# Kernel tuning notes

Hardware: AMD Instinct MI355X
Metric: run time of the kernel (lower is better)

The kernel has to match this reference:

```python
import jax, jax.numpy as jnp
import numpy as np

N_NODES = 50000
N_EDGES = 800000
IN_DIM = 256
OUT_DIM = 64
HEADS = 4
NEG_SLOPE = 0.2  # PyG GATConv default


def setup_inputs() -> dict:
    key = jax.random.key(0)
    k_x, k_e, k_w, k_as, k_ad = jax.random.split(key, 5)
    x = jax.random.normal(k_x, (N_NODES, IN_DIM), dtype=jnp.float32)
    edge_index = jax.random.randint(k_e, (2, N_EDGES), 0, N_NODES, dtype=jnp.int64)
    # Glorot-ish scaled params (as in PyG GATConv)
    W = jax.random.normal(k_w, (IN_DIM, HEADS * OUT_DIM), dtype=jnp.float32) / np.sqrt(IN_DIM)
    att_src = jax.random.normal(k_as, (HEADS, OUT_DIM), dtype=jnp.float32) / np.sqrt(OUT_DIM)
    att_dst = jax.random.normal(k_ad, (HEADS, OUT_DIM), dtype=jnp.float32) / np.sqrt(OUT_DIM)
    bias = jnp.zeros((HEADS * OUT_DIM,), dtype=jnp.float32)
    return {"x": x, "edge_index": edge_index, "W": W,
            "att_src": att_src, "att_dst": att_dst, "bias": bias}


def reference(x, edge_index, W, att_src, att_dst, bias):
    N = x.shape[0]
    H, C = att_src.shape
    # add self-loops (PyG GATConv default add_self_loops=True)
    loop = jnp.arange(N, dtype=edge_index.dtype)
    src = jnp.concatenate([edge_index[0], loop])  # [E+N] message sources j
    dst = jnp.concatenate([edge_index[1], loop])  # [E+N] message targets i

    xh = (x @ W).reshape(N, H, C)                 # [N, H, C]
    a_src = jnp.einsum('nhc,hc->nh', xh, att_src)  # [N, H]
    a_dst = jnp.einsum('nhc,hc->nh', xh, att_dst)  # [N, H]

    logits = jax.nn.leaky_relu(a_src[src] + a_dst[dst], NEG_SLOPE)  # [E+N, H]
    # segment softmax over incoming edges of each destination node
    seg_max = jax.ops.segment_max(logits, dst, num_segments=N)      # [N, H]
    e = jnp.exp(logits - seg_max[dst])
    seg_sum = jax.ops.segment_sum(e, dst, num_segments=N)           # [N, H]
    alpha = e / seg_sum[dst]                                        # [E+N, H]

    # weighted scatter-aggregate of source features
    msgs = alpha[:, :, None] * xh[src]                              # [E+N, H, C]
    out = jax.ops.segment_sum(msgs, dst, num_segments=N)            # [N, H, C]
    out = out.reshape(N, H * C) + bias                              # concat heads + bias
    # h.dim() == 2 here, so the original's mean(dim=1) branch is not taken
    return out
```

## Files before the change

kernel.cpp:

```cpp
#include <hip/hip_runtime.h>

#define NEG_SLOPE 0.2f
#define LRELU(x) ((x) > 0.0f ? (x) : NEG_SLOPE * (x))

typedef short short8 __attribute__((ext_vector_type(8)));
typedef unsigned short ushort8 __attribute__((ext_vector_type(8)));
typedef float f32x4v __attribute__((ext_vector_type(4)));

__device__ __forceinline__ unsigned short f2bf(float f) {
  unsigned int u = __float_as_uint(f);
  unsigned int r = (u + 0x7FFFu + ((u >> 16) & 1u)) >> 16;
  return (unsigned short)r;
}

__device__ __forceinline__ float bf2f(unsigned short u) {
  return __uint_as_float(((unsigned int)u) << 16);
}

__device__ __forceinline__ unsigned int cvt_pk_bf16(float lo, float hi) {
  unsigned int r;
  asm("v_cvt_pk_bf16_f32 %0, %1, %2" : "=v"(r) : "v"(lo), "v"(hi));
  return r;
}

__device__ __forceinline__ void gload_lds16(const void* g, void* l) {
  __builtin_amdgcn_global_load_lds(
      (const __attribute__((address_space(1))) unsigned int*)g,
      (__attribute__((address_space(3))) unsigned int*)l, 16, 0, 0);
}

#define CBC 448
#define CBW 64
#define CBF 1024

__global__ __launch_bounds__(256) void fused_pre(
    const float* __restrict__ W, unsigned short* __restrict__ Wtb,
    const int* __restrict__ ei, int* __restrict__ deg,
    int* __restrict__ rank, int E) {
  int b = blockIdx.x;
  int tid = threadIdx.x;
  if (b < CBC) {
    for (int e = b * 256 + tid; e < E; e += CBC * 256)
      rank[e] = atomicAdd(&deg[ei[E + e]], 1);
  } else {
    int bb = b - CBC;
    for (int idx = bb * 256 + tid; idx < 256 * 256; idx += CBW * 256) {
      int n = idx >> 8, k = idx & 255;
      Wtb[n * 256 + k] = f2bf(W[k * 256 + n]);
    }
  }
}

__global__ __launch_bounds__(1024) void scan1_kernel(const int* __restrict__ deg,
                                                     int* __restrict__ row_start,
                                                     int* __restrict__ bsum, int N) {
  __shared__ int buf[1024];
  int i = blockIdx.x * 1024 + (int)threadIdx.x;
  int v = (i < N) ? deg[i] : 0;
  buf[threadIdx.x] = v;
  __syncthreads();
  int run = v;
  for (int off = 1; off < 1024; off <<= 1) {
    int t = ((int)threadIdx.x >= off) ? buf[threadIdx.x - off] : 0;
    __syncthreads();
    run += t;
    buf[threadIdx.x] = run;
    __syncthreads();
  }
  if (i < N) row_start[i] = run - v;
  if (threadIdx.x == 1023) bsum[blockIdx.x] = run;
}

__global__ __launch_bounds__(1024) void scan_off(int* __restrict__ row_start,
                                                 const int* __restrict__ bsum,
                                                 int nb, int N) {
  __shared__ int s_off;
  int b = blockIdx.x;
  if (threadIdx.x < 64) {
    int acc = 0;
    for (int j = (int)threadIdx.x; j < b; j += 64) acc += bsum[j];
    for (int off = 32; off; off >>= 1) acc += __shfl_down(acc, off, 64);
    if (threadIdx.x == 0) s_off = acc;
  }
  __syncthreads();
  int off = s_off;
  int i = b * 1024 + (int)threadIdx.x;
  if (i < N) row_start[i] += off;
  if (b == nb - 1 && threadIdx.x == 0) row_start[N] = off + bsum[b];
}

__global__ __launch_bounds__(256) void fused_main(
    const float* __restrict__ Xf, const unsigned short* __restrict__ Wtb,
    const float* __restrict__ attS, const float* __restrict__ attD,
    unsigned short* __restrict__ XHb, float* __restrict__ a_src,
    float* __restrict__ a_dst,
    const int* __restrict__ ei, const int* __restrict__ row_start,
    const int* __restrict__ rank, int* __restrict__ csr_src,
    int nGemm, int E, int N) {
  __shared__ unsigned short lA[128 * 32];
  __shared__ unsigned short lB[128 * 32];
  const int bid = blockIdx.x;
  const int tid = threadIdx.x;

  if (bid >= nGemm) {
    int bb = bid - nGemm;
    for (int e = bb * 256 + tid; e < E; e += CBF * 256)
      csr_src[row_start[ei[E + e]] + rank[e]] = ei[e];
    return;
  }

  const int gb = bid;
  const int lane = tid & 63;
  const int wave = tid >> 6;
  const int m0 = ((gb >> 4) * 8 + (gb & 7)) * 128;
  const int n0 = ((gb >> 3) & 1) * 128;
  const int wr = (wave >> 1) * 64;
  const int wc = (wave & 1) * 64;

  f32x4v acc[4][4];
#pragma unroll
  for (int i = 0; i < 4; ++i)
#pragma unroll
    for (int j = 0; j < 4; ++j) acc[i][j] = (f32x4v)(0.0f);

  const int srow = tid >> 2;
  const int skb = (tid & 3) * 16;
  const float* ap0 = Xf + (size_t)min(m0 + (tid >> 2), N - 1) * 256 + (tid & 3) * 8;
  const float* ap1 = Xf + (size_t)min(m0 + 64 + (tid >> 2), N - 1) * 256 + (tid & 3) * 8;

  const char* WtC = (const char*)Wtb;
  char* lAc = (char*)&lA[0];
  char* lBc = (char*)&lB[0];
  const int ldsB0 = wave * 1024;
  const int lr = lane & 15;
  const int hq = lane >> 4;
  const int kq = hq * 16;

  float4 c0 = *reinterpret_cast<const float4*>(ap0);
  float4 c1 = *reinterpret_cast<const float4*>(ap0 + 4);
  float4 c2 = *reinterpret_cast<const float4*>(ap1);
  float4 c3 = *reinterpret_cast<const float4*>(ap1 + 4);

#pragma unroll
  for (int kk = 0; kk < 8; ++kk) {
    const int k0 = kk * 32;
    gload_lds16(WtC + (size_t)(n0 + srow) * 512 + (size_t)k0 * 2 + skb, lBc + ldsB0);
    gload_lds16(WtC + (size_t)(n0 + srow + 64) * 512 + (size_t)k0 * 2 + skb,
                lBc + ldsB0 + 4096);
    {
      uint4 w0, w1;
      w0.x = cvt_pk_bf16(c0.x, c0.y); w0.y = cvt_pk_bf16(c0.z, c0.w);
      w0.z = cvt_pk_bf16(c1.x, c1.y); w0.w = cvt_pk_bf16(c1.z, c1.w);
      w1.x = cvt_pk_bf16(c2.x, c2.y); w1.y = cvt_pk_bf16(c2.z, c2.w);
      w1.z = cvt_pk_bf16(c3.x, c3.y); w1.w = cvt_pk_bf16(c3.z, c3.w);
      *reinterpret_cast<uint4*>(lAc + tid * 16) = w0;
      *reinterpret_cast<uint4*>(lAc + 4096 + tid * 16) = w1;
    }
    if (kk < 7) {
      c0 = *reinterpret_cast<const float4*>(ap0 + k0 + 32);
      c1 = *reinterpret_cast<const float4*>(ap0 + k0 + 36);
      c2 = *reinterpret_cast<const float4*>(ap1 + k0 + 32);
      c3 = *reinterpret_cast<const float4*>(ap1 + k0 + 36);
    }
    __syncthreads();

    short8 a[4], b[4];
#pragma unroll
    for (int i = 0; i < 4; ++i)
      a[i] = *reinterpret_cast<const short8*>(lAc + (wr + i * 16 + lr) * 64 + kq);
#pragma unroll
    for (int j = 0; j < 4; ++j)
      b[j] = *reinterpret_cast<const short8*>(lBc + (wc + j * 16 + lr) * 64 + kq);
#pragma unroll
    for (int i = 0; i < 4; ++i)
#pragma unroll
      for (int j = 0; j < 4; ++j)
        acc[i][j] = __builtin_amdgcn_mfma_f32_16x16x32_bf16(a[i], b[j], acc[i][j], 0, 0, 0);
    __syncthreads();
  }

  const int h = (n0 + wc) >> 6;
  float ws_[4], wd_[4];
#pragma unroll
  for (int j = 0; j < 4; ++j) {
    ws_[j] = attS[h * 64 + j * 16 + lr];
    wd_[j] = attD[h * 64 + j * 16 + lr];
  }
  const int rbase = m0 + wr + hq * 4;

#pragma unroll
  for (int i = 0; i < 4; ++i) {
#pragma unroll
    for (int r = 0; r < 4; ++r) {
      float ps = 0.f, pd = 0.f;
#pragma unroll
      for (int j = 0; j < 4; ++j) {
        ps += acc[i][j][r] * ws_[j];
        pd += acc[i][j][r] * wd_[j];
      }
#pragma unroll
      for (int off = 1; off < 16; off <<= 1) {
        ps += __shfl_xor(ps, off, 64);
        pd += __shfl_xor(pd, off, 64);
      }
      int row = rbase + i * 16 + r;
      if (lr == 0 && row < N) {
        a_src[row * 4 + h] = ps;
        a_dst[row * 4 + h] = pd;
      }
    }
  }

#pragma unroll
  for (int i = 0; i < 4; ++i)
#pragma unroll
    for (int j = 0; j < 4; ++j) {
      int col = n0 + wc + j * 16 + lr;
#pragma unroll
      for (int r = 0; r < 4; ++r)
        XHb[(size_t)(rbase + i * 16 + r) * 256 + col] = f2bf(acc[i][j][r]);
    }
}

__global__ __launch_bounds__(256) void gat_agg(
    const unsigned short* __restrict__ XHb, const float* __restrict__ a_src,
    const float* __restrict__ a_dst, const int* __restrict__ row_start,
    const int* __restrict__ csr_src, const float* __restrict__ bias,
    float* __restrict__ out, int N) {
  int wid = threadIdx.x >> 6;
  int lane = threadIdx.x & 63;
  int node = blockIdx.x * 4 + wid;
  if (node >= N) return;

  const int half = lane >> 5;
  const int l5 = lane & 31;
  const int h = l5 >> 3;
  const int c = l5 << 3;
  const unsigned short* __restrict__ xrow = XHb + c;

  float ad_h = a_dst[node * 4 + h];
  float as_h = a_src[node * 4 + h];

  int start = row_start[node];
  int end = row_start[node + 1];

  float acc[8];
  float sw = 0.f;
  if (half == 0) {
    float wself = __expf(LRELU(as_h + ad_h));
    ushort8 sv = *reinterpret_cast<const ushort8*>(xrow + (size_t)node * 256);
#pragma unroll
    for (int k = 0; k < 8; ++k) acc[k] = wself * bf2f(sv[k]);
    sw = wself;
  } else {
#pragma unroll
    for (int k = 0; k < 8; ++k) acc[k] = 0.f;
  }

  int p = start;
  for (; p + 8 <= end; p += 8) {
    int s0 = csr_src[p + half];
    int s1 = csr_src[p + 2 + half];
    int s2 = csr_src[p + 4 + half];
    int s3 = csr_src[p + 6 + half];
    float a0 = a_src[s0 * 4 + h] + ad_h;
    float a1 = a_src[s1 * 4 + h] + ad_h;
    float a2 = a_src[s2 * 4 + h] + ad_h;
    float a3 = a_src[s3 * 4 + h] + ad_h;
    ushort8 u0 = *reinterpret_cast<const ushort8*>(xrow + (size_t)s0 * 256);
    ushort8 u1 = *reinterpret_cast<const ushort8*>(xrow + (size_t)s1 * 256);
    ushort8 u2 = *reinterpret_cast<const ushort8*>(xrow + (size_t)s2 * 256);
    ushort8 u3 = *reinterpret_cast<const ushort8*>(xrow + (size_t)s3 * 256);
    float w0 = __expf(LRELU(a0));
    float w1 = __expf(LRELU(a1));
    float w2 = __expf(LRELU(a2));
    float w3 = __expf(LRELU(a3));
#pragma unroll
    for (int k = 0; k < 8; ++k) {
      acc[k] += w0 * bf2f(u0[k]);
      acc[k] += w1 * bf2f(u1[k]);
      acc[k] += w2 * bf2f(u2[k]);
      acc[k] += w3 * bf2f(u3[k]);
    }
    sw += (w0 + w1) + (w2 + w3);
  }
#pragma unroll
  for (int k = 0; k < 4; ++k) {
    int idx = p + 2 * k + half;
    if (idx < end) {
      int s = csr_src[idx];
      float aa = a_src[s * 4 + h] + ad_h;
      ushort8 u = *reinterpret_cast<const ushort8*>(xrow + (size_t)s * 256);
      float ww = __expf(LRELU(aa));
#pragma unroll
      for (int q = 0; q < 8; ++q) acc[q] += ww * bf2f(u[q]);
      sw += ww;
    }
  }

  sw += __shfl_xor(sw, 32, 64);
#pragma unroll
  for (int k = 0; k < 8; ++k) acc[k] += __shfl_xor(acc[k], 32, 64);

  if (half == 0) {
    float inv = 1.0f / sw;
    float4 b0 = *reinterpret_cast<const float4*>(bias + c);
    float4 b1 = *reinterpret_cast<const float4*>(bias + c + 4);
    float4 o0, o1;
    o0.x = acc[0] * inv + b0.x; o0.y = acc[1] * inv + b0.y;
    o0.z = acc[2] * inv + b0.z; o0.w = acc[3] * inv + b0.w;
    o1.x = acc[4] * inv + b1.x; o1.y = acc[5] * inv + b1.y;
    o1.z = acc[6] * inv + b1.z; o1.w = acc[7] * inv + b1.w;
    *reinterpret_cast<float4*>(out + (size_t)node * 256 + c) = o0;
    *reinterpret_cast<float4*>(out + (size_t)node * 256 + c + 4) = o1;
  }
}

extern "C" void kernel_launch(void* const* d_in, const int* in_sizes, int n_in,
                              void* d_out, int out_size, void* d_ws, size_t ws_size,
                              hipStream_t stream) {
  const float* x    = (const float*)d_in[0];
  const int*   ei   = (const int*)d_in[1];
  const float* Wm   = (const float*)d_in[2];
  const float* attS = (const float*)d_in[3];
  const float* attD = (const float*)d_in[4];
  const float* bias = (const float*)d_in[5];
  float* out = (float*)d_out;

  const int N = in_sizes[0] / 256;
  const int E = in_sizes[1] / 2;
  const int Mp = (N + 1023) / 1024 * 1024;
  const int nb = (N + 1023) / 1024;

  char* w = (char*)d_ws;
  unsigned short* XHb = (unsigned short*)w;  w += (size_t)Mp * 256 * 2;
  unsigned short* Wtb = (unsigned short*)w;  w += (size_t)256 * 256 * 2;
  float* a_src = (float*)w;                  w += (size_t)N * 4 * 4;
  float* a_dst = (float*)w;                  w += (size_t)N * 4 * 4;
  int* deg = (int*)w;                        w += (size_t)N * 4;
  int* rank = (int*)w;                       w += (size_t)E * 4;
  int* row_start = (int*)w;                  w += ((size_t)(N + 1) * 4 + 255) / 256 * 256;
  int* bsum = (int*)w;                       w += ((size_t)nb * 4 + 255) / 256 * 256;
  int* csr_src = (int*)w;                    w += (size_t)E * 4;

  hipMemsetAsync(deg, 0, (size_t)N * 4, stream);

  fused_pre<<<CBC + CBW, 256, 0, stream>>>(Wm, Wtb, ei, deg, rank, E);

  scan1_kernel<<<nb, 1024, 0, stream>>>(deg, row_start, bsum, N);
  scan_off<<<nb, 1024, 0, stream>>>(row_start, bsum, nb, N);

  const int nGemm = 2 * (Mp / 128);
  fused_main<<<nGemm + CBF, 256, 0, stream>>>(x, Wtb, attS, attD, XHb, a_src, a_dst,
                                              ei, row_start, rank, csr_src,
                                              nGemm, E, N);

  gat_agg<<<(N + 3) / 4, 256, 0, stream>>>(XHb, a_src, a_dst, row_start, csr_src,
                                           bias, out, N);
}
```

Measured before the change: 148.7 us.

## Replace two-pass scan with atomic block offsets; stage full W tile in LDS for GEMM

The two-kernel prefix scan becomes one kernel. Each block grabs its base offset with an atomicAdd on a global counter, so CSR segments are placed in arbitrary block order, and the aggregation kernel now computes each row end as start + deg. The GEMM now loads the whole 128x256 bf16 W slice into XOR-swizzled LDS once. Each wave reads its A fragments straight from global fp32 and converts them in registers, which removes the per-k-step LDS staging and barriers. The cost is 64KB of LDS per block, which may limit occupancy, and unbuffered global A loads inside the k loop.

```diff
diff --git a/kernel.cpp b/kernel.cpp
--- a/kernel.cpp
+++ b/kernel.cpp
@@ -51,10 +51,11 @@
   }
 }
 
-__global__ __launch_bounds__(1024) void scan1_kernel(const int* __restrict__ deg,
-                                                     int* __restrict__ row_start,
-                                                     int* __restrict__ bsum, int N) {
+__global__ __launch_bounds__(1024) void scan_alloc(const int* __restrict__ deg,
+                                                   int* __restrict__ row_start,
+                                                   int* __restrict__ gtotal, int N) {
   __shared__ int buf[1024];
+  __shared__ int s_off;
   int i = blockIdx.x * 1024 + (int)threadIdx.x;
   int v = (i < N) ? deg[i] : 0;
   buf[threadIdx.x] = v;
@@ -67,26 +68,9 @@
     buf[threadIdx.x] = run;
     __syncthreads();
   }
-  if (i < N) row_start[i] = run - v;
-  if (threadIdx.x == 1023) bsum[blockIdx.x] = run;
-}
-
-__global__ __launch_bounds__(1024) void scan_off(int* __restrict__ row_start,
-                                                 const int* __restrict__ bsum,
-                                                 int nb, int N) {
-  __shared__ int s_off;
-  int b = blockIdx.x;
-  if (threadIdx.x < 64) {
-    int acc = 0;
-    for (int j = (int)threadIdx.x; j < b; j += 64) acc += bsum[j];
-    for (int off = 32; off; off >>= 1) acc += __shfl_down(acc, off, 64);
-    if (threadIdx.x == 0) s_off = acc;
-  }
+  if (threadIdx.x == 1023) s_off = atomicAdd(gtotal, run);
   __syncthreads();
-  int off = s_off;
-  int i = b * 1024 + (int)threadIdx.x;
-  if (i < N) row_start[i] += off;
-  if (b == nb - 1 && threadIdx.x == 0) row_start[N] = off + bsum[b];
+  if (i < N) row_start[i] = s_off + run - v;
 }
 
 __global__ __launch_bounds__(256) void fused_main(
@@ -97,8 +81,7 @@
     const int* __restrict__ ei, const int* __restrict__ row_start,
     const int* __restrict__ rank, int* __restrict__ csr_src,
     int nGemm, int E, int N) {
-  __shared__ unsigned short lA[128 * 32];
-  __shared__ unsigned short lB[128 * 32];
+  __shared__ unsigned short lB[128 * 256];
   const int bid = blockIdx.x;
   const int tid = threadIdx.x;
 
@@ -114,119 +97,123 @@
   const int wave = tid >> 6;
   const int m0 = ((gb >> 4) * 8 + (gb & 7)) * 128;
   const int n0 = ((gb >> 3) & 1) * 128;
-  const int wr = (wave >> 1) * 64;
-  const int wc = (wave & 1) * 64;
-
-  f32x4v acc[4][4];
-#pragma unroll
-  for (int i = 0; i < 4; ++i)
-#pragma unroll
-    for (int j = 0; j < 4; ++j) acc[i][j] = (f32x4v)(0.0f);
-
-  const int srow = tid >> 2;
-  const int skb = (tid & 3) * 16;
-  const float* ap0 = Xf + (size_t)min(m0 + (tid >> 2), N - 1) * 256 + (tid & 3) * 8;
-  const float* ap1 = Xf + (size_t)min(m0 + 64 + (tid >> 2), N - 1) * 256 + (tid & 3) * 8;
-
-  const char* WtC = (const char*)Wtb;
-  char* lAc = (char*)&lA[0];
-  char* lBc = (char*)&lB[0];
-  const int ldsB0 = wave * 1024;
   const int lr = lane & 15;
   const int hq = lane >> 4;
-  const int kq = hq * 16;
-
-  float4 c0 = *reinterpret_cast<const float4*>(ap0);
-  float4 c1 = *reinterpret_cast<const float4*>(ap0 + 4);
-  float4 c2 = *reinterpret_cast<const float4*>(ap1);
-  float4 c3 = *reinterpret_cast<const float4*>(ap1 + 4);
+
+  char* lBc = (char*)&lB[0];
+  const char* WtC = (const char*)Wtb;
+
+#pragma unroll
+  for (int is = 0; is < 16; ++is) {
+    int off = is * 4096 + wave * 1024 + lane * 16;
+    int row = off >> 9;
+    int within = off & 511;
+    int g = (off & ~511) | (within ^ ((row & 7) << 4));
+    gload_lds16(WtC + (size_t)n0 * 512 + g, lBc + is * 4096 + wave * 1024);
+  }
+
+  f32x4v acc[2][8];
+#pragma unroll
+  for (int i = 0; i < 2; ++i)
+#pragma unroll
+    for (int j = 0; j < 8; ++j) acc[i][j] = (f32x4v)(0.0f);
+
+  const int r0 = min(m0 + wave * 32 + lr, N - 1);
+  const int r1 = min(m0 + wave * 32 + 16 + lr, N - 1);
+  const float* ap0 = Xf + (size_t)r0 * 256 + hq * 8;
+  const float* ap1 = Xf + (size_t)r1 * 256 + hq * 8;
+  const int sw = (lr & 7) << 4;
+
+  __syncthreads();
 
 #pragma unroll
   for (int kk = 0; kk < 8; ++kk) {
     const int k0 = kk * 32;
-    gload_lds16(WtC + (size_t)(n0 + srow) * 512 + (size_t)k0 * 2 + skb, lBc + ldsB0);
-    gload_lds16(WtC + (size_t)(n0 + srow + 64) * 512 + (size_t)k0 * 2 + skb,
-                lBc + ldsB0 + 4096);
+    short8 a[2], b[8];
     {
-      uint4 w0, w1;
-      w0.x = cvt_pk_bf16(c0.x, c0.y); w0.y = cvt_pk_bf16(c0.z, c0.w);
-      w0.z = cvt_pk_bf16(c1.x, c1.y); w0.w = cvt_pk_bf16(c1.z, c1.w);
-      w1.x = cvt_pk_bf16(c2.x, c2.y); w1.y = cvt_pk_bf16(c2.z, c2.w);
-      w1.z = cvt_pk_bf16(c3.x, c3.y); w1.w = cvt_pk_bf16(c3.z, c3.w);
-      *reinterpret_cast<uint4*>(lAc + tid * 16) = w0;
-      *reinterpret_cast<uint4*>(lAc + 4096 + tid * 16) = w1;
-    }
-    if (kk < 7) {
-      c0 = *reinterpret_cast<const float4*>(ap0 + k0 + 32);
-      c1 = *reinterpret_cast<const float4*>(ap0 + k0 + 36);
-      c2 = *reinterpret_cast<const float4*>(ap1 + k0 + 32);
-      c3 = *reinterpret_cast<const float4*>(ap1 + k0 + 36);
-    }
-    __syncthreads();
-
-    short8 a[4], b[4];
-#pragma unroll
-    for (int i = 0; i < 4; ++i)
-      a[i] = *reinterpret_cast<const short8*>(lAc + (wr + i * 16 + lr) * 64 + kq);
-#pragma unroll
-    for (int j = 0; j < 4; ++j)
-      b[j] = *reinterpret_cast<const short8*>(lBc + (wc + j * 16 + lr) * 64 + kq);
-#pragma unroll
-    for (int i = 0; i < 4; ++i)
-#pragma unroll
-      for (int j = 0; j < 4; ++j)
+      float4 f00 = *reinterpret_cast<const float4*>(ap0 + k0);
+      float4 f01 = *reinterpret_cast<const float4*>(ap0 + k0 + 4);
+      float4 f10 = *reinterpret_cast<const float4*>(ap1 + k0);
+      float4 f11 = *reinterpret_cast<const float4*>(ap1 + k0 + 4);
+      union { unsigned int u[4]; short8 s; } ua0, ua1;
+      ua0.u[0] = cvt_pk_bf16(f00.x, f00.y);
+      ua0.u[1] = cvt_pk_bf16(f00.z, f00.w);
+      ua0.u[2] = cvt_pk_bf16(f01.x, f01.y);
+      ua0.u[3] = cvt_pk_bf16(f01.z, f01.w);
+      ua1.u[0] = cvt_pk_bf16(f10.x, f10.y);
+      ua1.u[1] = cvt_pk_bf16(f10.z, f10.w);
+      ua1.u[2] = cvt_pk_bf16(f11.x, f11.y);
+      ua1.u[3] = cvt_pk_bf16(f11.z, f11.w);
+      a[0] = ua0.s;
+      a[1] = ua1.s;
+    }
+    const int cbyte = (k0 * 2 + hq * 16) ^ sw;
+#pragma unroll
+    for (int j = 0; j < 8; ++j)
+      b[j] = *reinterpret_cast<const short8*>(lBc + (j * 16 + lr) * 512 + cbyte);
+#pragma unroll
+    for (int i = 0; i < 2; ++i)
+#pragma unroll
+      for (int j = 0; j < 8; ++j)
         acc[i][j] = __builtin_amdgcn_mfma_f32_16x16x32_bf16(a[i], b[j], acc[i][j], 0, 0, 0);
-    __syncthreads();
-  }
-
-  const int h = (n0 + wc) >> 6;
-  float ws_[4], wd_[4];
-#pragma unroll
-  for (int j = 0; j < 4; ++j) {
-    ws_[j] = attS[h * 64 + j * 16 + lr];
-    wd_[j] = attD[h * 64 + j * 16 + lr];
-  }
-  const int rbase = m0 + wr + hq * 4;
-
-#pragma unroll
-  for (int i = 0; i < 4; ++i) {
+  }
+
+  const int h0 = n0 >> 6;
+  float ws_[8], wd_[8];
+#pragma unroll
+  for (int j = 0; j < 8; ++j) {
+    ws_[j] = attS[(h0 + (j >> 2)) * 64 + (j & 3) * 16 + lr];
+    wd_[j] = attD[(h0 + (j >> 2)) * 64 + (j & 3) * 16 + lr];
+  }
+  const int rbase = m0 + wave * 32 + hq * 4;
+
+#pragma unroll
+  for (int i = 0; i < 2; ++i) {
 #pragma unroll
     for (int r = 0; r < 4; ++r) {
-      float ps = 0.f, pd = 0.f;
+      float ps0 = 0.f, pd0 = 0.f, ps1 = 0.f, pd1 = 0.f;
 #pragma unroll
       for (int j = 0; j < 4; ++j) {
-        ps += acc[i][j][r] * ws_[j];
-        pd += acc[i][j][r] * wd_[j];
+        ps0 += acc[i][j][r] * ws_[j];
+        pd0 += acc[i][j][r] * wd_[j];
+        ps1 += acc[i][j + 4][r] * ws_[j + 4];
+        pd1 += acc[i][j + 4][r] * wd_[j + 4];
       }
 #pragma unroll
       for (int off = 1; off < 16; off <<= 1) {
-        ps += __shfl_xor(ps, off, 64);
-        pd += __shfl_xor(pd, off, 64);
+        ps0 += __shfl_xor(ps0, off, 64);
+        pd0 += __shfl_xor(pd0, off, 64);
+        ps1 += __shfl_xor(ps1, off, 64);
+        pd1 += __shfl_xor(pd1, off, 64);
       }
       int row = rbase + i * 16 + r;
       if (lr == 0 && row < N) {
-        a_src[row * 4 + h] = ps;
-        a_dst[row * 4 + h] = pd;
+        a_src[row * 4 + h0] = ps0;
+        a_dst[row * 4 + h0] = pd0;
+        a_src[row * 4 + h0 + 1] = ps1;
+        a_dst[row * 4 + h0 + 1] = pd1;
       }
     }
   }
 
 #pragma unroll
-  for (int i = 0; i < 4; ++i)
-#pragma unroll
-    for (int j = 0; j < 4; ++j) {
-      int col = n0 + wc + j * 16 + lr;
-#pragma unroll
-      for (int r = 0; r < 4; ++r)
-        XHb[(size_t)(rbase + i * 16 + r) * 256 + col] = f2bf(acc[i][j][r]);
+  for (int i = 0; i < 2; ++i)
+#pragma unroll
+    for (int j = 0; j < 8; ++j) {
+      int col = n0 + j * 16 + lr;
+#pragma unroll
+      for (int r = 0; r < 4; ++r) {
+        int row = rbase + i * 16 + r;
+        XHb[(size_t)row * 256 + col] = f2bf(acc[i][j][r]);
+      }
     }
 }
 
 __global__ __launch_bounds__(256) void gat_agg(
     const unsigned short* __restrict__ XHb, const float* __restrict__ a_src,
     const float* __restrict__ a_dst, const int* __restrict__ row_start,
-    const int* __restrict__ csr_src, const float* __restrict__ bias,
-    float* __restrict__ out, int N) {
+    const int* __restrict__ deg, const int* __restrict__ csr_src,
+    const float* __restrict__ bias, float* __restrict__ out, int N) {
   int wid = threadIdx.x >> 6;
   int lane = threadIdx.x & 63;
   int node = blockIdx.x * 4 + wid;
@@ -242,7 +229,7 @@
   float as_h = a_src[node * 4 + h];
 
   int start = row_start[node];
-  int end = row_start[node + 1];
+  int end = start + deg[node];
 
   float acc[8];
   float sw = 0.f;
@@ -338,23 +325,22 @@
   float* a_src = (float*)w;                  w += (size_t)N * 4 * 4;
   float* a_dst = (float*)w;                  w += (size_t)N * 4 * 4;
   int* deg = (int*)w;                        w += (size_t)N * 4;
+  int* gtotal = (int*)w;                     w += 256;
   int* rank = (int*)w;                       w += (size_t)E * 4;
   int* row_start = (int*)w;                  w += ((size_t)(N + 1) * 4 + 255) / 256 * 256;
-  int* bsum = (int*)w;                       w += ((size_t)nb * 4 + 255) / 256 * 256;
   int* csr_src = (int*)w;                    w += (size_t)E * 4;
 
-  hipMemsetAsync(deg, 0, (size_t)N * 4, stream);
+  hipMemsetAsync(deg, 0, (size_t)N * 4 + 256, stream);
 
   fused_pre<<<CBC + CBW, 256, 0, stream>>>(Wm, Wtb, ei, deg, rank, E);
 
-  scan1_kernel<<<nb, 1024, 0, stream>>>(deg, row_start, bsum, N);
-  scan_off<<<nb, 1024, 0, stream>>>(row_start, bsum, nb, N);
+  scan_alloc<<<nb, 1024, 0, stream>>>(deg, row_start, gtotal, N);
 
   const int nGemm = 2 * (Mp / 128);
   fused_main<<<nGemm + CBF, 256, 0, stream>>>(x, Wtb, attS, attD, XHb, a_src, a_dst,
                                               ei, row_start, rank, csr_src,
                                               nGemm, E, N);
 
-  gat_agg<<<(N + 3) / 4, 256, 0, stream>>>(XHb, a_src, a_dst, row_start, csr_src,
-                                           bias, out, N);
-}
+  gat_agg<<<(N + 3) / 4, 256, 0, stream>>>(XHb, a_src, a_dst, row_start, deg,
+                                           csr_src, bias, out, N);
+}
```

After: 148.1 us. About the same (-0.4%).
